# Kernel tuning notes

Hardware: AMD Instinct MI355X
Metric: run time of the kernel (lower is better)

Reference implementation:

```python
import jax, jax.numpy as jnp
import numpy as np

B, S, D, H = 2, 2048, 1024, 16
DH = D // H
EPS = 1e-5
LAMBDA_INIT = 0.8


def setup_inputs() -> dict:
    key = jax.random.key(0)
    ks = jax.random.split(key, 16)
    w_std = 1.0 / np.sqrt(D)
    lam_std = LAMBDA_INIT / np.sqrt(DH)
    return {
        "x": jax.random.normal(ks[0], (B, S, D), jnp.float32),
        # Linear weights stored [in, out] (y = x @ W + b), equivalent to torch W.T
        "Wq": jax.random.normal(ks[1], (D, D), jnp.float32) * w_std,
        "bq": jax.random.normal(ks[2], (D,), jnp.float32) * 0.02,
        "Wk": jax.random.normal(ks[3], (D, D), jnp.float32) * w_std,
        "bk": jax.random.normal(ks[4], (D,), jnp.float32) * 0.02,
        "Wv": jax.random.normal(ks[5], (D, D), jnp.float32) * w_std,
        "bv": jax.random.normal(ks[6], (D,), jnp.float32) * 0.02,
        "Wo": jax.random.normal(ks[7], (D, D), jnp.float32) * w_std,
        "bo": jax.random.normal(ks[8], (D,), jnp.float32) * 0.02,
        "lq1": jax.random.normal(ks[9], (H, DH), jnp.float32) * lam_std,
        "lk1": jax.random.normal(ks[10], (H, DH), jnp.float32) * lam_std,
        "lq2": jax.random.normal(ks[11], (H, DH), jnp.float32) * lam_std,
        "lk2": jax.random.normal(ks[12], (H, DH), jnp.float32) * lam_std,
        # per-head GroupNorm(1, head_dim) affine params (torch default init)
        "gn_w": jnp.ones((H, DH), jnp.float32),
        "gn_b": jnp.zeros((H, DH), jnp.float32),
    }


def reference(x, Wq, bq, Wk, bk, Wv, bv, Wo, bo, lq1, lk1, lq2, lk2, gn_w, gn_b):
    b, s, d = x.shape
    h, dh = lq1.shape
    scale = dh ** -0.5

    q = (x @ Wq + bq).reshape(b, s, h, dh)
    k = (x @ Wk + bk).reshape(b, s, h, dh)
    v = (x @ Wv + bv).reshape(b, s, h, dh)

    # differential lambda per head: exp(<lq1,lk1>) - exp(<lq2,lk2>) + lambda_init
    lam = jnp.exp((lq1 * lk1).sum(-1)) - jnp.exp((lq2 * lk2).sum(-1)) + LAMBDA_INIT  # [H]

    scores = jnp.einsum("bihd,bjhd->bhij", q, k) * scale * lam[None, :, None, None]
    attn = jax.nn.softmax(scores, axis=-1)  # no mask in default call path
    out = jnp.einsum("bhij,bjhd->bihd", attn, v)  # [B,S,H,DH]

    # per-head GroupNorm(1, head_dim): normalize over (seq, head_dim) per (batch, head)
    mean = out.mean(axis=(1, 3), keepdims=True)
    var = out.var(axis=(1, 3), keepdims=True)
    normed = (out - mean) * jax.lax.rsqrt(var + EPS)
    normed = normed * gn_w[None, None, :, :] + gn_b[None, None, :, :]

    y = normed.reshape(b, s, d) @ Wo + bo
    return y
```

## Files before the change

### kernel.cpp

```cpp
#include <hip/hip_runtime.h>

#define S_LEN 2048
#define D_DIM 1024
#define H_NUM 16
#define DH 64
#define EPS_GN 1e-5f
#define LAMBDA_INIT 0.8f

typedef unsigned short bfu;
typedef __attribute__((ext_vector_type(8))) short bf16x8;
typedef __attribute__((ext_vector_type(4))) float f32x4;

union FragU { uint4 u; bf16x8 f; };

__device__ inline float bf2f(bfu u){
  union { unsigned int i; float f; } c; c.i = ((unsigned int)u) << 16; return c.f;
}
__device__ inline bfu f2bf(float f){
  union { float f; unsigned int u; } c; c.f = f;
  unsigned int r = c.u + 0x7fffu + ((c.u >> 16) & 1u);
  return (bfu)(r >> 16);
}
__device__ inline unsigned cvtpk(float lo, float hi){
  unsigned r;
  asm("v_cvt_pk_bf16_f32 %0, %1, %2" : "=v"(r) : "v"(lo), "v"(hi));
  return r;
}
__device__ inline float ldx(const void* p, size_t i, int isf32){
  return isf32 ? ((const float*)p)[i] : bf2f(((const bfu*)p)[i]);
}
__device__ inline float wave_sum(float x){
  #pragma unroll
  for (int off = 32; off; off >>= 1) x += __shfl_xor(x, off, 64);
  return x;
}

__global__ void lambda_kernel(const void* __restrict__ lq1, const void* __restrict__ lk1,
                              const void* __restrict__ lq2, const void* __restrict__ lk2,
                              const unsigned int* __restrict__ gnw_bits,
                              int* __restrict__ flag, float* __restrict__ lam,
                              float* __restrict__ sums){
  const int isf32 = (gnw_bits[0] == 0x3F800000u) ? 1 : 0;
  int t = threadIdx.x;
  if (t == 0) flag[0] = isf32;
  sums[t] = 0.f;
  if (t < H_NUM){
    float s1 = 0.f, s2 = 0.f;
    for (int d = 0; d < DH; ++d){
      s1 += ldx(lq1, t*DH+d, isf32) * ldx(lk1, t*DH+d, isf32);
      s2 += ldx(lq2, t*DH+d, isf32) * ldx(lk2, t*DH+d, isf32);
    }
    lam[t] = expf(s1) - expf(s2) + LAMBDA_INIT;
  }
}

__global__ __launch_bounds__(256) void prep_all(
    const void* __restrict__ x,
    const void* __restrict__ w0, const void* __restrict__ w1,
    const void* __restrict__ w2, const void* __restrict__ w3,
    const int* __restrict__ flag, bfu* __restrict__ xb, bfu* __restrict__ wt)
{
  const int isf32 = flag[0];
  if (blockIdx.x < 2048){
    size_t i = ((size_t)blockIdx.x * 256 + threadIdx.x) * 8;
    if (isf32){
      const float* xf = (const float*)x;
      float4 a = *(const float4*)(xf + i);
      float4 b = *(const float4*)(xf + i + 4);
      bfu o[8] = {f2bf(a.x),f2bf(a.y),f2bf(a.z),f2bf(a.w),f2bf(b.x),f2bf(b.y),f2bf(b.z),f2bf(b.w)};
      *(uint4*)(xb + i) = *(const uint4*)o;
    } else {
      *(uint4*)(xb + i) = *(const uint4*)((const bfu*)x + i);
    }
    return;
  }
  const int widx = blockIdx.x - 2048;
  const int wsel = widx >> 8, tile = widx & 255;
  const void* W = (wsel==0)?w0:(wsel==1)?w1:(wsel==2)?w2:w3;
  bfu* dst = wt + (size_t)wsel * D_DIM * D_DIM;
  __shared__ float Ts[64][65];
  const int r0 = (tile >> 4) * 64, c0 = (tile & 15) * 64;
  const int ty = threadIdx.x >> 6, tx = threadIdx.x & 63;
  #pragma unroll
  for (int rr = 0; rr < 16; ++rr){
    int row = ty*16 + rr;
    Ts[row][tx] = ldx(W, (size_t)(r0 + row) * D_DIM + c0 + tx, isf32);
  }
  __syncthreads();
  #pragma unroll
  for (int rr = 0; rr < 16; ++rr){
    int row = ty*16 + rr;
    dst[(size_t)(c0 + row) * D_DIM + r0 + tx] = f2bf(Ts[tx][row]);
  }
}

__global__ __launch_bounds__(256) void qkv_mfma(
    const bfu* __restrict__ xb, const bfu* __restrict__ wt,
    const void* __restrict__ bq, const void* __restrict__ bk, const void* __restrict__ bv,
    const float* __restrict__ lam, const int* __restrict__ flag,
    bfu* __restrict__ qb, bfu* __restrict__ kb, bfu* __restrict__ vt)
{
  const int isf32 = flag[0];
  const int z = blockIdx.z;
  const bfu* Wt = wt + (size_t)z * D_DIM * D_DIM;
  const void* bias = (z==0)?bq:(z==1)?bk:bv;

  __shared__ __align__(16) ushort As[128][40];
  __shared__ __align__(16) ushort Bs[128][40];
  const int m0 = blockIdx.x * 128, n0 = blockIdx.y * 128;
  const int t = threadIdx.x, w = t >> 6, lane = t & 63;
  const int quad = lane >> 4, l15 = lane & 15;
  const int mbase = (w >> 1) * 64, nbase = (w & 1) * 64;
  const int srow = t >> 1, shalf = (t & 1) * 16;

  f32x4 acc[4][4];
  #pragma unroll
  for (int i = 0; i < 4; ++i)
    #pragma unroll
    for (int j = 0; j < 4; ++j){ f32x4 zz = {0.f,0.f,0.f,0.f}; acc[i][j] = zz; }

  for (int k0 = 0; k0 < D_DIM; k0 += 32){
    const bfu* asrc = xb + (size_t)(m0 + srow) * D_DIM + k0 + shalf;
    const bfu* bsrc = Wt + (size_t)(n0 + srow) * D_DIM + k0 + shalf;
    uint4 a0 = *(const uint4*)asrc, a1 = *(const uint4*)(asrc + 8);
    uint4 b0 = *(const uint4*)bsrc, b1 = *(const uint4*)(bsrc + 8);
    *(uint4*)&As[srow][shalf]     = a0;  *(uint4*)&As[srow][shalf + 8] = a1;
    *(uint4*)&Bs[srow][shalf]     = b0;  *(uint4*)&Bs[srow][shalf + 8] = b1;
    __syncthreads();
    FragU af[4], bf[4];
    #pragma unroll
    for (int mt = 0; mt < 4; ++mt) af[mt].u = *(const uint4*)&As[mbase + mt*16 + l15][quad*8];
    #pragma unroll
    for (int nt = 0; nt < 4; ++nt) bf[nt].u = *(const uint4*)&Bs[nbase + nt*16 + l15][quad*8];
    #pragma unroll
    for (int mt = 0; mt < 4; ++mt)
      #pragma unroll
      for (int nt = 0; nt < 4; ++nt)
        acc[mt][nt] = __builtin_amdgcn_mfma_f32_16x16x32_bf16(af[mt].f, bf[nt].f, acc[mt][nt], 0, 0, 0);
    __syncthreads();
  }

  #pragma unroll
  for (int mt = 0; mt < 4; ++mt){
    const int mrow = m0 + mbase + mt*16 + quad*4;
    #pragma unroll
    for (int nt = 0; nt < 4; ++nt){
      const int n = n0 + nbase + nt*16 + l15;
      const float bn = ldx(bias, n, isf32);
      if (z < 2){
        bfu* out = (z == 0) ? qb : kb;
        const float qs = (z == 0) ? 0.18033688f * lam[n >> 6] : 1.0f;
        #pragma unroll
        for (int r = 0; r < 4; ++r)
          out[(size_t)(mrow + r) * D_DIM + n] = f2bf((acc[mt][nt][r] + bn) * qs);
      } else {
        const int b = mrow >> 11, s = mrow & (S_LEN - 1);
        const int h = n >> 6, d = n & 63;
        ushort4 pk;
        pk.x = f2bf(acc[mt][nt][0] + bn); pk.y = f2bf(acc[mt][nt][1] + bn);
        pk.z = f2bf(acc[mt][nt][2] + bn); pk.w = f2bf(acc[mt][nt][3] + bn);
        *(ushort4*)(vt + (((size_t)(b*H_NUM + h)*DH + d)*S_LEN) + s) = pk;
      }
    }
  }
}

__global__ __launch_bounds__(256) void repack_k(const bfu* __restrict__ kb, bfu* __restrict__ ksw){
  __shared__ __align__(16) ushort L[64][72];
  const int b = blockIdx.z, h = blockIdx.y, j0 = blockIdx.x * 64;
  const int t = threadIdx.x;
  const int bh = b*H_NUM + h;
  {
    const int j = t >> 2, seg = (t & 3) * 16;
    const bfu* src = kb + ((size_t)(b*S_LEN + j0 + j)*H_NUM + h)*DH + seg;
    uint4 a = *(const uint4*)src, c = *(const uint4*)(src + 8);
    *(uint4*)&L[j][seg] = a; *(uint4*)&L[j][seg+8] = c;
  }
  __syncthreads();
  #pragma unroll
  for (int half = 0; half < 2; ++half){
    int c16 = half*256 + t;
    int blk = c16 >> 6;
    int l   = c16 & 63;
    int jt = blk >> 1, c = blk & 1;
    int m = l & 15, q = l >> 4;
    uint4 v = *(const uint4*)&L[jt*16 + m][c*32 + q*8];
    bfu* dst = ksw + (((size_t)bh*128 + (j0>>4) + jt)*2 + c)*512 + (size_t)l*8;
    *(uint4*)dst = v;
  }
}

__global__ __launch_bounds__(256) void repack_v(const bfu* __restrict__ vt, bfu* __restrict__ vsw){
  __shared__ __align__(16) ushort L[64][72];
  const int b = blockIdx.z, h = blockIdx.y, j0 = blockIdx.x * 64;
  const int t = threadIdx.x;
  const int bh = b*H_NUM + h;
  {
    const int d = t >> 2, seg = (t & 3) * 16;
    const bfu* src = vt + ((size_t)bh*DH + d)*S_LEN + j0 + seg;
    uint4 a = *(const uint4*)src, c = *(const uint4*)(src + 8);
    *(uint4*)&L[d][seg] = a; *(uint4*)&L[d][seg+8] = c;
  }
  __syncthreads();
  #pragma unroll
  for (int half = 0; half < 2; ++half){
    int c16 = half*256 + t;
    int blk = c16 >> 6;
    int l   = c16 & 63;
    int dt = blk >> 1, jcl = blk & 1;
    int m = l & 15, q = l >> 4;
    const int jb = jcl*32 + 16*(q>>1) + 4*(q&1);
    uint2 v0 = *(const uint2*)&L[dt*16 + m][jb];
    uint2 v1 = *(const uint2*)&L[dt*16 + m][jb + 8];
    uint4 v; v.x = v0.x; v.y = v0.y; v.z = v1.x; v.w = v1.y;
    bfu* dst = vsw + (((size_t)bh*4 + dt)*64 + (j0>>5) + jcl)*512 + (size_t)l*8;
    *(uint4*)dst = v;
  }
}

__global__ __launch_bounds__(256, 2) void attn_mfma(
    const bfu* __restrict__ qb, const bfu* __restrict__ ksw, const bfu* __restrict__ vsw,
    bfu* __restrict__ o)
{
  const int b = blockIdx.z, h = blockIdx.y, i0 = blockIdx.x * 128;
  const int t = threadIdx.x, w = t >> 6, lane = t & 63;
  const int quad = lane >> 4, l15 = lane & 15;
  const int bh = b*H_NUM + h;

  FragU qf[2][2];
  #pragma unroll
  for (int mt = 0; mt < 2; ++mt){
    const bfu* qrow = qb + ((size_t)(b*S_LEN + i0 + w*32 + mt*16 + l15)*H_NUM + h)*DH;
    qf[mt][0].u = *(const uint4*)(qrow + quad*8);
    qf[mt][1].u = *(const uint4*)(qrow + 32 + quad*8);
  }

  const bfu* kbase = ksw + (size_t)bh*131072 + (size_t)lane*8;
  const bfu* vbase = vsw + (size_t)bh*131072 + (size_t)lane*8;

  f32x4 Oacc[2][4];
  #pragma unroll
  for (int mt = 0; mt < 2; ++mt)
    #pragma unroll
    for (int dt = 0; dt < 4; ++dt){ f32x4 zz = {0.f,0.f,0.f,0.f}; Oacc[mt][dt] = zz; }
  float lsum[2] = {0.f, 0.f};

  FragU kfA[4][2], vfA[2][4], kfB[4][2], vfB[2][4];

#define LOAD_K(KF, J0)                                                          \
  { _Pragma("unroll")                                                           \
    for (int jt = 0; jt < 4; ++jt){                                             \
      const bfu* kr = kbase + (size_t)(((J0)>>4) + jt)*1024;                    \
      KF[jt][0].u = *(const uint4*)kr;                                          \
      KF[jt][1].u = *(const uint4*)(kr + 512);                                  \
    } }
#define LOAD_V(VF, J0)                                                          \
  { _Pragma("unroll")                                                           \
    for (int jt2 = 0; jt2 < 2; ++jt2)                                           \
      _Pragma("unroll")                                                         \
      for (int dt = 0; dt < 4; ++dt)                                            \
        VF[jt2][dt].u = *(const uint4*)(vbase + (size_t)(dt*64 + ((J0)>>5) + jt2)*512); }

#define PROCESS(KF, VF)                                                         \
  {                                                                             \
    f32x4 s[2][4];                                                              \
    _Pragma("unroll")                                                           \
    for (int jt = 0; jt < 4; ++jt){                                             \
      _Pragma("unroll")                                                         \
      for (int mt = 0; mt < 2; ++mt){                                           \
        f32x4 zz = {0.f,0.f,0.f,0.f};                                           \
        zz = __builtin_amdgcn_mfma_f32_16x16x32_bf16(KF[jt][0].f, qf[mt][0].f, zz, 0, 0, 0); \
        zz = __builtin_amdgcn_mfma_f32_16x16x32_bf16(KF[jt][1].f, qf[mt][1].f, zz, 0, 0, 0); \
        s[mt][jt] = zz;                                                         \
      }                                                                         \
    }                                                                           \
    _Pragma("unroll")                                                           \
    for (int mt = 0; mt < 2; ++mt){                                             \
      float ps = 0.f;                                                           \
      _Pragma("unroll")                                                         \
      for (int jt = 0; jt < 4; ++jt){                                           \
        _Pragma("unroll")                                                       \
        for (int r = 0; r < 4; ++r){                                            \
          float p = __builtin_exp2f(s[mt][jt][r]);                              \
          s[mt][jt][r] = p;                                                     \
          ps += p;                                                              \
        }                                                                       \
      }                                                                         \
      lsum[mt] += ps;                                                           \
      _Pragma("unroll")                                                         \
      for (int jt2 = 0; jt2 < 2; ++jt2){                                        \
        unsigned pa0 = cvtpk(s[mt][2*jt2][0],   s[mt][2*jt2][1]);               \
        unsigned pa1 = cvtpk(s[mt][2*jt2][2],   s[mt][2*jt2][3]);               \
        unsigned pb0 = cvtpk(s[mt][2*jt2+1][0], s[mt][2*jt2+1][1]);             \
        unsigned pb1 = cvtpk(s[mt][2*jt2+1][2], s[mt][2*jt2+1][3]);             \
        auto r0 = __builtin_amdgcn_permlane32_swap(pa0, pb0, false, false);     \
        auto r1 = __builtin_amdgcn_permlane32_swap(pa1, pb1, false, false);     \
        FragU pf;                                                               \
        pf.u.x = r0[0]; pf.u.y = r1[0]; pf.u.z = r0[1]; pf.u.w = r1[1];         \
        _Pragma("unroll")                                                       \
        for (int dt = 0; dt < 4; ++dt)                                          \
          Oacc[mt][dt] = __builtin_amdgcn_mfma_f32_16x16x32_bf16(VF[jt2][dt].f, pf.f, Oacc[mt][dt], 0, 0, 0); \
      }                                                                         \
    }                                                                           \
  }

  LOAD_K(kfA, 0)
  LOAD_V(vfA, 0)
  for (int j0 = 0; j0 < S_LEN; j0 += 128){
    LOAD_K(kfB, j0 + 64)
    LOAD_V(vfB, j0 + 64)
    PROCESS(kfA, vfA)
    if (j0 + 128 < S_LEN){
      LOAD_K(kfA, j0 + 128)
      LOAD_V(vfA, j0 + 128)
    }
    PROCESS(kfB, vfB)
  }
#undef LOAD_K
#undef LOAD_V
#undef PROCESS

  #pragma unroll
  for (int mt = 0; mt < 2; ++mt){
    float l = lsum[mt];
    l += __shfl_xor(l, 16, 64);
    l += __shfl_xor(l, 32, 64);
    float inv = 1.f / l;
    bfu* orow = o + ((size_t)(b*S_LEN + i0 + w*32 + mt*16 + l15)*H_NUM + h)*DH;
    #pragma unroll
    for (int dt = 0; dt < 4; ++dt){
      ushort4 pk;
      pk.x = f2bf(Oacc[mt][dt][0]*inv); pk.y = f2bf(Oacc[mt][dt][1]*inv);
      pk.z = f2bf(Oacc[mt][dt][2]*inv); pk.w = f2bf(Oacc[mt][dt][3]*inv);
      *(ushort4*)(orow + dt*16 + quad*4) = pk;
    }
  }
}

__global__ __launch_bounds__(256) void gn_part(const bfu* __restrict__ o, float* __restrict__ sums){
  const int bh = blockIdx.x >> 3, chunk = blockIdx.x & 7;
  const int b = bh >> 4, h = bh & 15;
  const bfu* base = o + ((size_t)(b*S_LEN + chunk*256)*H_NUM + h)*DH;
  float s1 = 0.f, s2 = 0.f;
  for (int u = threadIdx.x*4; u < 256*64; u += 256*4){
    int s = u >> 6, d = u & 63;
    ushort4 p = *(const ushort4*)(base + (size_t)s * D_DIM + d);
    float v0 = bf2f(p.x), v1 = bf2f(p.y), v2 = bf2f(p.z), v3 = bf2f(p.w);
    s1 += v0+v1+v2+v3; s2 += v0*v0+v1*v1+v2*v2+v3*v3;
  }
  s1 = wave_sum(s1); s2 = wave_sum(s2);
  __shared__ float r1[4], r2[4];
  int w = threadIdx.x >> 6, lane = threadIdx.x & 63;
  if (lane == 0){ r1[w] = s1; r2[w] = s2; }
  __syncthreads();
  if (threadIdx.x == 0){
    atomicAdd(&sums[bh*2+0], r1[0]+r1[1]+r1[2]+r1[3]);
    atomicAdd(&sums[bh*2+1], r2[0]+r2[1]+r2[2]+r2[3]);
  }
}

__global__ __launch_bounds__(256) void gn_fold(
    const bfu* __restrict__ wt,
    const void* __restrict__ bo, const float* __restrict__ sums,
    const void* __restrict__ gnw, const void* __restrict__ gnb,
    const int* __restrict__ flag,
    bfu* __restrict__ wt2, float* __restrict__ beta)
{
  const int isf32 = flag[0];
  const int z = blockIdx.y;
  const int t = threadIdx.x;
  const int n = blockIdx.x*16 + (t >> 4);
  const int seg = t & 15;
  const float invN = 1.f / (float)(S_LEN * DH);
  const float s1 = sums[(z*H_NUM + seg)*2], s2 = sums[(z*H_NUM + seg)*2 + 1];
  const float mu = s1 * invN;
  const float ri = rsqrtf(s2 * invN - mu*mu + EPS_GN);
  const bfu* src = wt + (size_t)n * D_DIM + seg*64;
  bfu* dst = wt2 + (size_t)z * D_DIM * D_DIM + (size_t)n * D_DIM + seg*64;
  float bacc = 0.f;
  #pragma unroll
  for (int i0 = 0; i0 < 64; i0 += 8){
    uint4 wv = *(const uint4*)(src + i0);
    const bfu* wp = (const bfu*)&wv;
    bfu outv[8];
    #pragma unroll
    for (int j = 0; j < 8; ++j){
      const int c = seg*64 + i0 + j;
      const float wq = bf2f(wp[j]);
      const float a = ri * ldx(gnw, c, isf32);
      outv[j] = f2bf(wq * a);
      bacc += (ldx(gnb, c, isf32) - mu * a) * wq;
    }
    *(uint4*)(dst + i0) = *(const uint4*)outv;
  }
  #pragma unroll
  for (int off = 1; off < 16; off <<= 1) bacc += __shfl_xor(bacc, off, 64);
  if (seg == 0) beta[z*D_DIM + n] = bacc + ldx(bo, n, isf32);
}

__global__ __launch_bounds__(256) void oproj_mfma(
    const bfu* __restrict__ ob, const bfu* __restrict__ wt2,
    const float* __restrict__ beta, const int* __restrict__ flag, void* __restrict__ y)
{
  const int isf32 = flag[0];
  __shared__ __align__(16) ushort As[64][40];
  __shared__ __align__(16) ushort Bs[128][40];
  const int m0 = blockIdx.x * 64, n0 = blockIdx.y * 128;
  const int t = threadIdx.x, w = t >> 6, lane = t & 63;
  const int quad = lane >> 4, l15 = lane & 15;
  const int mbase = (w >> 1) * 32, nbase = (w & 1) * 64;
  const int bB = m0 >> 11;
  const bfu* Wt = wt2 + (size_t)bB * D_DIM * D_DIM;
  const float* bet = beta + bB * D_DIM;

  const int arow = t >> 2, aseg = (t & 3) * 8;
  const int brow = t >> 1, bhalf = (t & 1) * 16;

  f32x4 acc[2][4];
  #pragma unroll
  for (int i = 0; i < 2; ++i)
    #pragma unroll
    for (int j = 0; j < 4; ++j){ f32x4 zz = {0.f,0.f,0.f,0.f}; acc[i][j] = zz; }

  for (int k0 = 0; k0 < D_DIM; k0 += 32){
    *(uint4*)&As[arow][aseg] = *(const uint4*)(ob + (size_t)(m0 + arow) * D_DIM + k0 + aseg);
    const bfu* bsrc = Wt + (size_t)(n0 + brow) * D_DIM + k0 + bhalf;
    uint4 b0 = *(const uint4*)bsrc, b1 = *(const uint4*)(bsrc + 8);
    *(uint4*)&Bs[brow][bhalf]     = b0;  *(uint4*)&Bs[brow][bhalf + 8] = b1;
    __syncthreads();
    FragU af[2], bfr[4];
    #pragma unroll
    for (int mt = 0; mt < 2; ++mt) af[mt].u = *(const uint4*)&As[mbase + mt*16 + l15][quad*8];
    #pragma unroll
    for (int nt = 0; nt < 4; ++nt) bfr[nt].u = *(const uint4*)&Bs[nbase + nt*16 + l15][quad*8];
    #pragma unroll
    for (int mt = 0; mt < 2; ++mt)
      #pragma unroll
      for (int nt = 0; nt < 4; ++nt)
        acc[mt][nt] = __builtin_amdgcn_mfma_f32_16x16x32_bf16(af[mt].f, bfr[nt].f, acc[mt][nt], 0, 0, 0);
    __syncthreads();
  }

  #pragma unroll
  for (int mt = 0; mt < 2; ++mt){
    const int mrow = m0 + mbase + mt*16 + quad*4;
    #pragma unroll
    for (int nt = 0; nt < 4; ++nt){
      const int n = n0 + nbase + nt*16 + l15;
      const float bn = bet[n];
      #pragma unroll
      for (int r = 0; r < 4; ++r){
        float val = acc[mt][nt][r] + bn;
        if (isf32) ((float*)y)[(size_t)(mrow + r) * D_DIM + n] = val;
        else       ((bfu*)y)[(size_t)(mrow + r) * D_DIM + n] = f2bf(val);
      }
    }
  }
}

extern "C" void kernel_launch(void* const* d_in, const int* in_sizes, int n_in,
                              void* d_out, int out_size, void* d_ws, size_t ws_size,
                              hipStream_t stream)
{
  const void* x   = d_in[0];
  const void* Wq  = d_in[1];
  const void* bq  = d_in[2];
  const void* Wk  = d_in[3];
  const void* bk  = d_in[4];
  const void* Wv  = d_in[5];
  const void* bv  = d_in[6];
  const void* Wo  = d_in[7];
  const void* bo  = d_in[8];
  const void* lq1 = d_in[9];
  const void* lk1 = d_in[10];
  const void* lq2 = d_in[11];
  const void* lk2 = d_in[12];
  const void* gnw = d_in[13];
  const void* gnb = d_in[14];

  float* ws   = (float*)d_ws;
  int*   flag = (int*)d_ws;
  float* lam  = ws + 16;
  float* sums = ws + 48;

  const size_t MB = 1u << 20;
  char* base = (char*)d_ws + 4096;
  bfu* xb  = (bfu*)(base);
  bfu* wt  = (bfu*)(base + 8*MB);
  bfu* qb  = (bfu*)(base + 16*MB);
  bfu* kb  = (bfu*)(base + 24*MB);
  bfu* vt  = (bfu*)(base + 32*MB);
  bfu* ob  = (bfu*)(base + 40*MB);
  bfu* ksw = xb;
  bfu* vsw = kb;
  bfu* wt2 = vt;
  float* beta = (float*)(base + 36*MB);

  lambda_kernel<<<1, 64, 0, stream>>>(lq1, lk1, lq2, lk2, (const unsigned int*)gnw, flag, lam, sums);
  prep_all<<<3072, 256, 0, stream>>>(x, Wq, Wk, Wv, Wo, flag, xb, wt);
  qkv_mfma<<<dim3(32, 8, 3), 256, 0, stream>>>(xb, wt, bq, bk, bv, lam, flag, qb, kb, vt);
  repack_k<<<dim3(32, 16, 2), 256, 0, stream>>>(kb, ksw);
  repack_v<<<dim3(32, 16, 2), 256, 0, stream>>>(vt, vsw);
  attn_mfma<<<dim3(16, 16, 2), 256, 0, stream>>>(qb, ksw, vsw, ob);
  gn_part<<<256, 256, 0, stream>>>(ob, sums);
  gn_fold<<<dim3(64, 2), 256, 0, stream>>>(wt + (size_t)3*D_DIM*D_DIM, bo, sums, gnw, gnb, flag, wt2, beta);
  oproj_mfma<<<dim3(64, 8), 256, 0, stream>>>(ob, wt2, beta, flag, d_out);
}
```

Baseline: 296.0 us.

## Double-buffer QKV GEMM tiles with direct global-to-LDS loads and XOR swizzle

Rewrites the QKV projection GEMM main loop to use global_load_lds (direct global-to-LDS DMA) into a two-stage LDS buffer. The next K tile is prefetched while MFMAs run on the current one. The padded LDS layout is replaced by an XOR-swizzled unpadded layout to avoid bank conflicts, and launch bounds request 3 blocks per CU. This targets global-load latency and register staging in the projection GEMM, at the cost of manual vmcnt waits and barrier correctness risks.

```diff
diff --git a/kernel.cpp b/kernel.cpp
--- a/kernel.cpp
+++ b/kernel.cpp
@@ -25,6 +25,11 @@
   unsigned r;
   asm("v_cvt_pk_bf16_f32 %0, %1, %2" : "=v"(r) : "v"(lo), "v"(hi));
   return r;
+}
+__device__ inline void gload16(const void* g, void* lds){
+  __builtin_amdgcn_global_load_lds(
+      (const __attribute__((address_space(1))) void*)g,
+      (__attribute__((address_space(3))) void*)lds, 16, 0, 0);
 }
 __device__ inline float ldx(const void* p, size_t i, int isf32){
   return isf32 ? ((const float*)p)[i] : bf2f(((const bfu*)p)[i]);
@@ -94,7 +99,7 @@
   }
 }
 
-__global__ __launch_bounds__(256) void qkv_mfma(
+__global__ __launch_bounds__(256, 3) void qkv_mfma(
     const bfu* __restrict__ xb, const bfu* __restrict__ wt,
     const void* __restrict__ bq, const void* __restrict__ bk, const void* __restrict__ bv,
     const float* __restrict__ lam, const int* __restrict__ flag,
@@ -105,13 +110,24 @@
   const bfu* Wt = wt + (size_t)z * D_DIM * D_DIM;
   const void* bias = (z==0)?bq:(z==1)?bk:bv;
 
-  __shared__ __align__(16) ushort As[128][40];
-  __shared__ __align__(16) ushort Bs[128][40];
+  __shared__ __align__(16) ushort As[2][128][32];
+  __shared__ __align__(16) ushort Bs[2][128][32];
   const int m0 = blockIdx.x * 128, n0 = blockIdx.y * 128;
   const int t = threadIdx.x, w = t >> 6, lane = t & 63;
   const int quad = lane >> 4, l15 = lane & 15;
   const int mbase = (w >> 1) * 64, nbase = (w & 1) * 64;
-  const int srow = t >> 1, shalf = (t & 1) * 16;
+
+  const int srow = w*32 + (lane >> 2);
+  const int gchunk = (lane & 3) ^ ((lane >> 3) & 3);
+  const size_t aoff = (size_t)(m0 + srow) * D_DIM + gchunk*8;
+  const size_t boff = (size_t)(n0 + srow) * D_DIM + gchunk*8;
+
+#define STAGE(buf, k0) {                                                  \
+    gload16(xb + aoff + (k0),            &As[buf][w*32][0]);              \
+    gload16(xb + aoff + 16*D_DIM + (k0), &As[buf][w*32+16][0]);           \
+    gload16(Wt + boff + (k0),            &Bs[buf][w*32][0]);              \
+    gload16(Wt + boff + 16*D_DIM + (k0), &Bs[buf][w*32+16][0]);           \
+  }
 
   f32x4 acc[4][4];
   #pragma unroll
@@ -119,26 +135,32 @@
     #pragma unroll
     for (int j = 0; j < 4; ++j){ f32x4 zz = {0.f,0.f,0.f,0.f}; acc[i][j] = zz; }
 
+  const int chq = (quad ^ ((l15 >> 1) & 3)) * 8;
+
+  STAGE(0, 0)
+  int buf = 0;
   for (int k0 = 0; k0 < D_DIM; k0 += 32){
-    const bfu* asrc = xb + (size_t)(m0 + srow) * D_DIM + k0 + shalf;
-    const bfu* bsrc = Wt + (size_t)(n0 + srow) * D_DIM + k0 + shalf;
-    uint4 a0 = *(const uint4*)asrc, a1 = *(const uint4*)(asrc + 8);
-    uint4 b0 = *(const uint4*)bsrc, b1 = *(const uint4*)(bsrc + 8);
-    *(uint4*)&As[srow][shalf]     = a0;  *(uint4*)&As[srow][shalf + 8] = a1;
-    *(uint4*)&Bs[srow][shalf]     = b0;  *(uint4*)&Bs[srow][shalf + 8] = b1;
-    __syncthreads();
+    if (k0 + 32 < D_DIM){
+      STAGE(buf ^ 1, k0 + 32)
+      asm volatile("s_waitcnt vmcnt(4)" ::: "memory");
+    } else {
+      asm volatile("s_waitcnt vmcnt(0)" ::: "memory");
+    }
+    __builtin_amdgcn_s_barrier();
     FragU af[4], bf[4];
     #pragma unroll
-    for (int mt = 0; mt < 4; ++mt) af[mt].u = *(const uint4*)&As[mbase + mt*16 + l15][quad*8];
-    #pragma unroll
-    for (int nt = 0; nt < 4; ++nt) bf[nt].u = *(const uint4*)&Bs[nbase + nt*16 + l15][quad*8];
+    for (int mt = 0; mt < 4; ++mt) af[mt].u = *(const uint4*)&As[buf][mbase + mt*16 + l15][chq];
+    #pragma unroll
+    for (int nt = 0; nt < 4; ++nt) bf[nt].u = *(const uint4*)&Bs[buf][nbase + nt*16 + l15][chq];
     #pragma unroll
     for (int mt = 0; mt < 4; ++mt)
       #pragma unroll
       for (int nt = 0; nt < 4; ++nt)
         acc[mt][nt] = __builtin_amdgcn_mfma_f32_16x16x32_bf16(af[mt].f, bf[nt].f, acc[mt][nt], 0, 0, 0);
-    __syncthreads();
-  }
+    __builtin_amdgcn_s_barrier();
+    buf ^= 1;
+  }
+#undef STAGE
 
   #pragma unroll
   for (int mt = 0; mt < 4; ++mt){
```

After: 271.4 us. 8.3% less time.
